# Kernel optimization log

Hardware: AMD Instinct MI355X
Metric: run time of the kernel (lower is better)

The kernel has to match this reference:

```python
import jax, jax.numpy as jnp
import numpy as np

EPS = 1e-5  # torch LayerNorm default

def layer_norm(x, g, b):
    m = jnp.mean(x)
    v = jnp.mean((x - m) ** 2)  # biased variance, as in torch LayerNorm
    return (x - m) * jax.lax.rsqrt(v + EPS) * g + b

def setup_inputs() -> dict:
    key = jax.random.key(0)
    ks = jax.random.split(key, 8)
    sz_I, sz_H1, sz_H2, sz_O = 2048, 4096, 4096, 1024
    def w(k, out_d, in_d):
        return jax.random.normal(k, (out_d, in_d), dtype=jnp.float32) / np.sqrt(in_d)
    return {
        "input_raw": jax.random.normal(ks[0], (sz_I,), dtype=jnp.float32),
        "h2_prev": jax.random.normal(ks[1], (sz_H2,), dtype=jnp.float32),
        "W_I_H1": w(ks[2], sz_H1, sz_I),
        "W_H2_H1": w(ks[3], sz_H1, sz_H2),
        "W_H1_H2": w(ks[4], sz_H2, sz_H1),
        "W_H1_O": w(ks[5], sz_O, sz_H1),
        "W_H2_O": w(ks[6], sz_O, sz_H2),
        "g_H1": jnp.ones((sz_H1,), jnp.float32), "b_H1": jnp.zeros((sz_H1,), jnp.float32),
        "g_H2": jnp.ones((sz_H2,), jnp.float32), "b_H2": jnp.zeros((sz_H2,), jnp.float32),
        "g_O": jnp.ones((sz_O,), jnp.float32), "b_O": jnp.zeros((sz_O,), jnp.float32),
    }

def reference(input_raw, h2_prev, W_I_H1, W_H2_H1, W_H1_H2, W_H1_O, W_H2_O,
              g_H1, b_H1, g_H2, b_H2, g_O, b_O):
    act = jnp.tanh
    # message: out_act(in_act(LN_target(W @ x))); with tanh/identity composed = tanh once
    def msg(W, x, g, b):
        return act(layer_norm(W @ x, g, b))
    i_out = input_raw                                   # I layer output
    h1 = msg(W_I_H1, i_out, g_H1, b_H1) + msg(W_H2_H1, h2_prev, g_H1, b_H1)
    h2 = msg(W_H1_H2, h1, g_H2, b_H2)
    o_acc = msg(W_H1_O, h1, g_O, b_O) + msg(W_H2_O, h2, g_O, b_O)
    # final output-layer activation: out_act(LN_O(acc))
    o_final = act(layer_norm(o_acc, g_O, b_O))
    return o_final
```

## Files before the change

### kernel.cpp

```cpp
#include <hip/hip_runtime.h>

#define LN_EPS 1e-5f

__device__ __forceinline__ float wave_sum(float v) {
    #pragma unroll
    for (int o = 32; o; o >>= 1) v += __shfl_down(v, o);
    return v;
}

__device__ __forceinline__ float block_sum_256(float v, float* sh) {
    int lane = threadIdx.x & 63, w = threadIdx.x >> 6;
    v = wave_sum(v);
    if (lane == 0) sh[w] = v;
    __syncthreads();
    float r = sh[0] + sh[1] + sh[2] + sh[3];
    __syncthreads();
    return r;
}

__device__ __forceinline__ float block_sum_1024(float v, float* sh) {
    int lane = threadIdx.x & 63, w = threadIdx.x >> 6;
    v = wave_sum(v);
    if (lane == 0) sh[w] = v;
    __syncthreads();
    if (w == 0) {
        float s = (lane < 16) ? sh[lane] : 0.f;
        #pragma unroll
        for (int o = 8; o; o >>= 1) s += __shfl_down(s, o);
        if (lane == 0) sh[0] = s;
    }
    __syncthreads();
    float r = sh[0];
    __syncthreads();
    return r;
}

__global__ __launch_bounds__(256) void k1(
        const float* __restrict__ W_I_H1, const float* __restrict__ x_in,
        const float* __restrict__ W_H2_H1, const float* __restrict__ h2_prev,
        float* __restrict__ t1, float* __restrict__ t2,
        float2* __restrict__ p1, float2* __restrict__ p2) {
    extern __shared__ float xs[];
    __shared__ float shy[4];
    const float* W; const float* x; float* y; float2* p; int C; int blk;
    if ((int)blockIdx.x < 1024) {
        W = W_I_H1;  x = x_in;    y = t1; p = p1; C = 2048; blk = blockIdx.x;
    } else {
        W = W_H2_H1; x = h2_prev; y = t2; p = p2; C = 4096; blk = blockIdx.x - 1024;
    }
    int n4 = C >> 2;
    float4* xs4 = (float4*)xs;
    for (int i = threadIdx.x; i < n4; i += 256)
        xs4[i] = ((const float4*)x)[i];
    __syncthreads();

    int wave = threadIdx.x >> 6, lane = threadIdx.x & 63;
    int row = blk * 4 + wave;
    const float4* Wr = (const float4*)(W + (size_t)row * C);
    float acc = 0.f;
    #pragma unroll 4
    for (int i = lane; i < n4; i += 64) {
        float4 w = Wr[i], v = xs4[i];
        acc += w.x * v.x + w.y * v.y + w.z * v.z + w.w * v.w;
    }
    acc = wave_sum(acc);
    if (lane == 0) { y[row] = acc; shy[wave] = acc; }
    __syncthreads();
    if (threadIdx.x == 0) {
        float s = 0.f, q = 0.f;
        #pragma unroll
        for (int i = 0; i < 4; i++) { float v = shy[i]; s += v; q += v * v; }
        p[blk] = make_float2(s, q);
    }
}

__global__ __launch_bounds__(256) void k2(
        const float* __restrict__ t1, const float* __restrict__ t2,
        const float2* __restrict__ p1, const float2* __restrict__ p2,
        const float* __restrict__ g, const float* __restrict__ b,
        const float* __restrict__ W_H1_H2, const float* __restrict__ W_H1_O,
        float* __restrict__ t3, float* __restrict__ t4,
        float2* __restrict__ p3, float2* __restrict__ p4) {
    extern __shared__ float xs[];
    __shared__ float shr[4];
    __shared__ float shy[4];

    float s1 = 0.f, q1 = 0.f, s2 = 0.f, q2 = 0.f;
    for (int i = threadIdx.x; i < 1024; i += 256) {
        float2 a = p1[i]; s1 += a.x; q1 += a.y;
        float2 c = p2[i]; s2 += c.x; q2 += c.y;
    }
    s1 = block_sum_256(s1, shr); q1 = block_sum_256(q1, shr);
    s2 = block_sum_256(s2, shr); q2 = block_sum_256(q2, shr);
    const float invN = 1.f / 4096.f;
    float m1 = s1 * invN, r1 = rsqrtf(fmaxf(q1 * invN - m1 * m1, 0.f) + LN_EPS);
    float m2 = s2 * invN, r2 = rsqrtf(fmaxf(q2 * invN - m2 * m2, 0.f) + LN_EPS);

    float4* xs4 = (float4*)xs;
    for (int i = threadIdx.x; i < 1024; i += 256) {
        float4 a = ((const float4*)t1)[i], c = ((const float4*)t2)[i];
        float4 gv = ((const float4*)g)[i], bv = ((const float4*)b)[i];
        float4 o;
        o.x = tanhf((a.x - m1) * r1 * gv.x + bv.x) + tanhf((c.x - m2) * r2 * gv.x + bv.x);
        o.y = tanhf((a.y - m1) * r1 * gv.y + bv.y) + tanhf((c.y - m2) * r2 * gv.y + bv.y);
        o.z = tanhf((a.z - m1) * r1 * gv.z + bv.z) + tanhf((c.z - m2) * r2 * gv.z + bv.z);
        o.w = tanhf((a.w - m1) * r1 * gv.w + bv.w) + tanhf((c.w - m2) * r2 * gv.w + bv.w);
        xs4[i] = o;
    }
    __syncthreads();

    const float* W; float* y; float2* p; int blk;
    if ((int)blockIdx.x < 1024) { W = W_H1_H2; y = t3; p = p3; blk = blockIdx.x; }
    else                        { W = W_H1_O;  y = t4; p = p4; blk = blockIdx.x - 1024; }
    int wave = threadIdx.x >> 6, lane = threadIdx.x & 63;
    int row = blk * 4 + wave;
    const float4* Wr = (const float4*)(W + (size_t)row * 4096);
    float acc = 0.f;
    #pragma unroll 4
    for (int i = lane; i < 1024; i += 64) {
        float4 w = Wr[i], v = xs4[i];
        acc += w.x * v.x + w.y * v.y + w.z * v.z + w.w * v.w;
    }
    acc = wave_sum(acc);
    if (lane == 0) { y[row] = acc; shy[wave] = acc; }
    __syncthreads();
    if (threadIdx.x == 0) {
        float s = 0.f, q = 0.f;
        #pragma unroll
        for (int i = 0; i < 4; i++) { float v = shy[i]; s += v; q += v * v; }
        p[blk] = make_float2(s, q);
    }
}

__global__ __launch_bounds__(256) void k3(
        const float* __restrict__ t3, const float2* __restrict__ p3,
        const float* __restrict__ g, const float* __restrict__ b,
        const float* __restrict__ W_H2_O,
        float* __restrict__ t5, float2* __restrict__ p5) {
    extern __shared__ float xs[];
    __shared__ float shr[4];
    __shared__ float shy[4];

    float s3 = 0.f, q3 = 0.f;
    for (int i = threadIdx.x; i < 1024; i += 256) {
        float2 a = p3[i]; s3 += a.x; q3 += a.y;
    }
    s3 = block_sum_256(s3, shr); q3 = block_sum_256(q3, shr);
    const float invN = 1.f / 4096.f;
    float m3 = s3 * invN, r3 = rsqrtf(fmaxf(q3 * invN - m3 * m3, 0.f) + LN_EPS);

    float4* xs4 = (float4*)xs;
    for (int i = threadIdx.x; i < 1024; i += 256) {
        float4 a = ((const float4*)t3)[i];
        float4 gv = ((const float4*)g)[i], bv = ((const float4*)b)[i];
        float4 o;
        o.x = tanhf((a.x - m3) * r3 * gv.x + bv.x);
        o.y = tanhf((a.y - m3) * r3 * gv.y + bv.y);
        o.z = tanhf((a.z - m3) * r3 * gv.z + bv.z);
        o.w = tanhf((a.w - m3) * r3 * gv.w + bv.w);
        xs4[i] = o;
    }
    __syncthreads();

    int wave = threadIdx.x >> 6, lane = threadIdx.x & 63;
    int row = blockIdx.x * 4 + wave;
    const float4* Wr = (const float4*)(W_H2_O + (size_t)row * 4096);
    float acc = 0.f;
    #pragma unroll 4
    for (int i = lane; i < 1024; i += 64) {
        float4 w = Wr[i], v = xs4[i];
        acc += w.x * v.x + w.y * v.y + w.z * v.z + w.w * v.w;
    }
    acc = wave_sum(acc);
    if (lane == 0) { t5[row] = acc; shy[wave] = acc; }
    __syncthreads();
    if (threadIdx.x == 0) {
        float s = 0.f, q = 0.f;
        #pragma unroll
        for (int i = 0; i < 4; i++) { float v = shy[i]; s += v; q += v * v; }
        p5[blockIdx.x] = make_float2(s, q);
    }
}

__global__ __launch_bounds__(1024) void k4(
        const float* __restrict__ t4, const float* __restrict__ t5,
        const float2* __restrict__ p4, const float2* __restrict__ p5,
        const float* __restrict__ g, const float* __restrict__ b,
        float* __restrict__ out) {
    __shared__ float sh[16];
    int tid = threadIdx.x;
    float a4 = 0.f, c4 = 0.f, a5 = 0.f, c5 = 0.f;
    if (tid < 256) {
        float2 v = p4[tid]; a4 = v.x; c4 = v.y;
        float2 w = p5[tid]; a5 = w.x; c5 = w.y;
    }
    float s4 = block_sum_1024(a4, sh), q4 = block_sum_1024(c4, sh);
    float s5 = block_sum_1024(a5, sh), q5 = block_sum_1024(c5, sh);
    const float invN = 1.f / 1024.f;
    float m4 = s4 * invN, r4 = rsqrtf(fmaxf(q4 * invN - m4 * m4, 0.f) + LN_EPS);
    float m5 = s5 * invN, r5 = rsqrtf(fmaxf(q5 * invN - m5 * m5, 0.f) + LN_EPS);

    float gi = g[tid], bi = b[tid];
    float o = tanhf((t4[tid] - m4) * r4 * gi + bi)
            + tanhf((t5[tid] - m5) * r5 * gi + bi);

    float s = block_sum_1024(o, sh), q = block_sum_1024(o * o, sh);
    float m = s * invN, r = rsqrtf(fmaxf(q * invN - m * m, 0.f) + LN_EPS);
    out[tid] = tanhf((o - m) * r * gi + bi);
}

extern "C" void kernel_launch(void* const* d_in, const int* in_sizes, int n_in,
                              void* d_out, int out_size, void* d_ws, size_t ws_size,
                              hipStream_t stream) {
    const float* input_raw = (const float*)d_in[0];
    const float* h2_prev   = (const float*)d_in[1];
    const float* W_I_H1    = (const float*)d_in[2];
    const float* W_H2_H1   = (const float*)d_in[3];
    const float* W_H1_H2   = (const float*)d_in[4];
    const float* W_H1_O    = (const float*)d_in[5];
    const float* W_H2_O    = (const float*)d_in[6];
    const float* g_H1 = (const float*)d_in[7],  *b_H1 = (const float*)d_in[8];
    const float* g_H2 = (const float*)d_in[9],  *b_H2 = (const float*)d_in[10];
    const float* g_O  = (const float*)d_in[11], *b_O  = (const float*)d_in[12];
    float* out = (float*)d_out;

    float* ws = (float*)d_ws;
    float*  t1 = ws;
    float*  t2 = ws + 4096;
    float*  t3 = ws + 8192;
    float*  t4 = ws + 12288;
    float*  t5 = ws + 13312;
    float2* p1 = (float2*)(ws + 14336);
    float2* p2 = (float2*)(ws + 16384);
    float2* p3 = (float2*)(ws + 18432);
    float2* p4 = (float2*)(ws + 20480);
    float2* p5 = (float2*)(ws + 20992);

    const size_t lds = 4096 * sizeof(float);

    k1<<<2048, 256, lds, stream>>>(W_I_H1, input_raw, W_H2_H1, h2_prev,
                                   t1, t2, p1, p2);
    k2<<<1280, 256, lds, stream>>>(t1, t2, p1, p2, g_H1, b_H1,
                                   W_H1_H2, W_H1_O, t3, t4, p3, p4);
    k3<<<256, 256, lds, stream>>>(t3, p3, g_H2, b_H2, W_H2_O, t5, p5);
    k4<<<1, 1024, 0, stream>>>(t4, t5, p4, p5, g_O, b_O, out);
}
```

Measured before the change: 237.3 us.

## Hoist LayerNorm+tanh into single-block kernels and split k3 rows across waves

Previously every GEMV block recomputed the LayerNorm statistics and the tanh of the whole 4096-element input vector, which is 1280 or 256 redundant copies. Now two single-block kernels compute h1 and h2 once and write them to workspace, and the GEMV kernels only copy the vector into LDS. k3 also splits each row across two waves and launches 512 blocks, which doubles the parallelism of that small GEMV. This costs two extra launches, each a serialized 1-block kernel, on a short critical path.

```diff
diff --git a/kernel.cpp b/kernel.cpp
--- a/kernel.cpp
+++ b/kernel.cpp
@@ -6,16 +6,6 @@
     #pragma unroll
     for (int o = 32; o; o >>= 1) v += __shfl_down(v, o);
     return v;
-}
-
-__device__ __forceinline__ float block_sum_256(float v, float* sh) {
-    int lane = threadIdx.x & 63, w = threadIdx.x >> 6;
-    v = wave_sum(v);
-    if (lane == 0) sh[w] = v;
-    __syncthreads();
-    float r = sh[0] + sh[1] + sh[2] + sh[3];
-    __syncthreads();
-    return r;
 }
 
 __device__ __forceinline__ float block_sum_1024(float v, float* sh) {
@@ -74,39 +64,40 @@
     }
 }
 
-__global__ __launch_bounds__(256) void k2(
+__global__ __launch_bounds__(1024) void ln2_add(
         const float* __restrict__ t1, const float* __restrict__ t2,
         const float2* __restrict__ p1, const float2* __restrict__ p2,
         const float* __restrict__ g, const float* __restrict__ b,
+        float* __restrict__ h1) {
+    __shared__ float sh[16];
+    int tid = threadIdx.x;
+    float2 a = p1[tid], c = p2[tid];
+    float s1 = block_sum_1024(a.x, sh), q1 = block_sum_1024(a.y, sh);
+    float s2 = block_sum_1024(c.x, sh), q2 = block_sum_1024(c.y, sh);
+    const float invN = 1.f / 4096.f;
+    float m1 = s1 * invN, r1 = rsqrtf(fmaxf(q1 * invN - m1 * m1, 0.f) + LN_EPS);
+    float m2 = s2 * invN, r2 = rsqrtf(fmaxf(q2 * invN - m2 * m2, 0.f) + LN_EPS);
+
+    float4 av = ((const float4*)t1)[tid], cv = ((const float4*)t2)[tid];
+    float4 gv = ((const float4*)g)[tid], bv = ((const float4*)b)[tid];
+    float4 o;
+    o.x = tanhf((av.x - m1) * r1 * gv.x + bv.x) + tanhf((cv.x - m2) * r2 * gv.x + bv.x);
+    o.y = tanhf((av.y - m1) * r1 * gv.y + bv.y) + tanhf((cv.y - m2) * r2 * gv.y + bv.y);
+    o.z = tanhf((av.z - m1) * r1 * gv.z + bv.z) + tanhf((cv.z - m2) * r2 * gv.z + bv.z);
+    o.w = tanhf((av.w - m1) * r1 * gv.w + bv.w) + tanhf((cv.w - m2) * r2 * gv.w + bv.w);
+    ((float4*)h1)[tid] = o;
+}
+
+__global__ __launch_bounds__(256) void k2(
+        const float* __restrict__ h1,
         const float* __restrict__ W_H1_H2, const float* __restrict__ W_H1_O,
         float* __restrict__ t3, float* __restrict__ t4,
         float2* __restrict__ p3, float2* __restrict__ p4) {
     extern __shared__ float xs[];
-    __shared__ float shr[4];
     __shared__ float shy[4];
-
-    float s1 = 0.f, q1 = 0.f, s2 = 0.f, q2 = 0.f;
-    for (int i = threadIdx.x; i < 1024; i += 256) {
-        float2 a = p1[i]; s1 += a.x; q1 += a.y;
-        float2 c = p2[i]; s2 += c.x; q2 += c.y;
-    }
-    s1 = block_sum_256(s1, shr); q1 = block_sum_256(q1, shr);
-    s2 = block_sum_256(s2, shr); q2 = block_sum_256(q2, shr);
-    const float invN = 1.f / 4096.f;
-    float m1 = s1 * invN, r1 = rsqrtf(fmaxf(q1 * invN - m1 * m1, 0.f) + LN_EPS);
-    float m2 = s2 * invN, r2 = rsqrtf(fmaxf(q2 * invN - m2 * m2, 0.f) + LN_EPS);
-
     float4* xs4 = (float4*)xs;
-    for (int i = threadIdx.x; i < 1024; i += 256) {
-        float4 a = ((const float4*)t1)[i], c = ((const float4*)t2)[i];
-        float4 gv = ((const float4*)g)[i], bv = ((const float4*)b)[i];
-        float4 o;
-        o.x = tanhf((a.x - m1) * r1 * gv.x + bv.x) + tanhf((c.x - m2) * r2 * gv.x + bv.x);
-        o.y = tanhf((a.y - m1) * r1 * gv.y + bv.y) + tanhf((c.y - m2) * r2 * gv.y + bv.y);
-        o.z = tanhf((a.z - m1) * r1 * gv.z + bv.z) + tanhf((c.z - m2) * r2 * gv.z + bv.z);
-        o.w = tanhf((a.w - m1) * r1 * gv.w + bv.w) + tanhf((c.w - m2) * r2 * gv.w + bv.w);
-        xs4[i] = o;
-    }
+    for (int i = threadIdx.x; i < 1024; i += 256)
+        xs4[i] = ((const float4*)h1)[i];
     __syncthreads();
 
     const float* W; float* y; float2* p; int blk;
@@ -132,53 +123,57 @@
     }
 }
 
-__global__ __launch_bounds__(256) void k3(
+__global__ __launch_bounds__(1024) void ln_tanh(
         const float* __restrict__ t3, const float2* __restrict__ p3,
         const float* __restrict__ g, const float* __restrict__ b,
-        const float* __restrict__ W_H2_O,
+        float* __restrict__ h2) {
+    __shared__ float sh[16];
+    int tid = threadIdx.x;
+    float2 a = p3[tid];
+    float s3 = block_sum_1024(a.x, sh), q3 = block_sum_1024(a.y, sh);
+    const float invN = 1.f / 4096.f;
+    float m3 = s3 * invN, r3 = rsqrtf(fmaxf(q3 * invN - m3 * m3, 0.f) + LN_EPS);
+
+    float4 av = ((const float4*)t3)[tid];
+    float4 gv = ((const float4*)g)[tid], bv = ((const float4*)b)[tid];
+    float4 o;
+    o.x = tanhf((av.x - m3) * r3 * gv.x + bv.x);
+    o.y = tanhf((av.y - m3) * r3 * gv.y + bv.y);
+    o.z = tanhf((av.z - m3) * r3 * gv.z + bv.z);
+    o.w = tanhf((av.w - m3) * r3 * gv.w + bv.w);
+    ((float4*)h2)[tid] = o;
+}
+
+__global__ __launch_bounds__(256) void k3(
+        const float* __restrict__ h2, const float* __restrict__ W_H2_O,
         float* __restrict__ t5, float2* __restrict__ p5) {
     extern __shared__ float xs[];
-    __shared__ float shr[4];
-    __shared__ float shy[4];
-
-    float s3 = 0.f, q3 = 0.f;
-    for (int i = threadIdx.x; i < 1024; i += 256) {
-        float2 a = p3[i]; s3 += a.x; q3 += a.y;
-    }
-    s3 = block_sum_256(s3, shr); q3 = block_sum_256(q3, shr);
-    const float invN = 1.f / 4096.f;
-    float m3 = s3 * invN, r3 = rsqrtf(fmaxf(q3 * invN - m3 * m3, 0.f) + LN_EPS);
-
+    __shared__ float shp[4];
     float4* xs4 = (float4*)xs;
-    for (int i = threadIdx.x; i < 1024; i += 256) {
-        float4 a = ((const float4*)t3)[i];
-        float4 gv = ((const float4*)g)[i], bv = ((const float4*)b)[i];
-        float4 o;
-        o.x = tanhf((a.x - m3) * r3 * gv.x + bv.x);
-        o.y = tanhf((a.y - m3) * r3 * gv.y + bv.y);
-        o.z = tanhf((a.z - m3) * r3 * gv.z + bv.z);
-        o.w = tanhf((a.w - m3) * r3 * gv.w + bv.w);
-        xs4[i] = o;
-    }
+    for (int i = threadIdx.x; i < 1024; i += 256)
+        xs4[i] = ((const float4*)h2)[i];
     __syncthreads();
 
     int wave = threadIdx.x >> 6, lane = threadIdx.x & 63;
-    int row = blockIdx.x * 4 + wave;
+    int row  = blockIdx.x * 2 + (wave >> 1);
+    int half = wave & 1;
     const float4* Wr = (const float4*)(W_H2_O + (size_t)row * 4096);
     float acc = 0.f;
-    #pragma unroll 4
-    for (int i = lane; i < 1024; i += 64) {
+    int i0 = half * 512 + lane;
+    #pragma unroll 8
+    for (int k = 0; k < 8; k++) {
+        int i = i0 + k * 64;
         float4 w = Wr[i], v = xs4[i];
         acc += w.x * v.x + w.y * v.y + w.z * v.z + w.w * v.w;
     }
     acc = wave_sum(acc);
-    if (lane == 0) { t5[row] = acc; shy[wave] = acc; }
+    if (lane == 0) shp[wave] = acc;
     __syncthreads();
     if (threadIdx.x == 0) {
-        float s = 0.f, q = 0.f;
-        #pragma unroll
-        for (int i = 0; i < 4; i++) { float v = shy[i]; s += v; q += v * v; }
-        p5[blockIdx.x] = make_float2(s, q);
+        float r0 = shp[0] + shp[1], r1 = shp[2] + shp[3];
+        t5[blockIdx.x * 2]     = r0;
+        t5[blockIdx.x * 2 + 1] = r1;
+        p5[blockIdx.x] = make_float2(r0 + r1, r0 * r0 + r1 * r1);
     }
 }
 
@@ -190,10 +185,8 @@
     __shared__ float sh[16];
     int tid = threadIdx.x;
     float a4 = 0.f, c4 = 0.f, a5 = 0.f, c5 = 0.f;
-    if (tid < 256) {
-        float2 v = p4[tid]; a4 = v.x; c4 = v.y;
-        float2 w = p5[tid]; a5 = w.x; c5 = w.y;
-    }
+    if (tid < 256) { float2 v = p4[tid]; a4 = v.x; c4 = v.y; }
+    if (tid < 512) { float2 w = p5[tid]; a5 = w.x; c5 = w.y; }
     float s4 = block_sum_1024(a4, sh), q4 = block_sum_1024(c4, sh);
     float s5 = block_sum_1024(a5, sh), q5 = block_sum_1024(c5, sh);
     const float invN = 1.f / 1024.f;
@@ -230,18 +223,21 @@
     float*  t3 = ws + 8192;
     float*  t4 = ws + 12288;
     float*  t5 = ws + 13312;
-    float2* p1 = (float2*)(ws + 14336);
-    float2* p2 = (float2*)(ws + 16384);
-    float2* p3 = (float2*)(ws + 18432);
-    float2* p4 = (float2*)(ws + 20480);
-    float2* p5 = (float2*)(ws + 20992);
+    float*  h1 = ws + 14336;
+    float*  h2 = ws + 18432;
+    float2* p1 = (float2*)(ws + 22528);
+    float2* p2 = (float2*)(ws + 24576);
+    float2* p3 = (float2*)(ws + 26624);
+    float2* p4 = (float2*)(ws + 28672);
+    float2* p5 = (float2*)(ws + 29184);
 
     const size_t lds = 4096 * sizeof(float);
 
     k1<<<2048, 256, lds, stream>>>(W_I_H1, input_raw, W_H2_H1, h2_prev,
                                    t1, t2, p1, p2);
-    k2<<<1280, 256, lds, stream>>>(t1, t2, p1, p2, g_H1, b_H1,
-                                   W_H1_H2, W_H1_O, t3, t4, p3, p4);
-    k3<<<256, 256, lds, stream>>>(t3, p3, g_H2, b_H2, W_H2_O, t5, p5);
+    ln2_add<<<1, 1024, 0, stream>>>(t1, t2, p1, p2, g_H1, b_H1, h1);
+    k2<<<1280, 256, lds, stream>>>(h1, W_H1_H2, W_H1_O, t3, t4, p3, p4);
+    ln_tanh<<<1, 1024, 0, stream>>>(t3, p3, g_H2, b_H2, h2);
+    k3<<<512, 256, lds, stream>>>(h2, W_H2_O, t5, p5);
     k4<<<1, 1024, 0, stream>>>(t4, t5, p4, p5, g_O, b_O, out);
 }
```

Result: no change. 237.5 us (+0.1%).
